# Kernel optimization log

Hardware: AMD Instinct MI355X
Metric: run time of the kernel (lower is better)

The kernel has to match this reference:

```python
import jax, jax.numpy as jnp
import numpy as np

EPS = 1e-5

def _ln(x, g, b):
    m = jnp.mean(x, axis=-1, keepdims=True)
    v = jnp.var(x, axis=-1, keepdims=True)
    return (x - m) * jax.lax.rsqrt(v + EPS) * g + b

def setup_inputs() -> dict:
    key = jax.random.key(0)
    ks = jax.random.split(key, 8)
    B, N, C, H = 2, 2048, 128, 8
    hid = 768
    s = lambda k, shp, fan: jax.random.normal(k, shp, jnp.float32) * (1.0 / np.sqrt(fan))
    return {
        "x1": jax.random.normal(ks[0], (B, N, C), jnp.float32),
        "x2": jax.random.normal(ks[1], (B, N, C), jnp.float32),
        "x3": jax.random.normal(ks[2], (B, N, C), jnp.float32),
        "ln1_g": jnp.ones((3, C), jnp.float32),
        "ln1_b": jnp.zeros((3, C), jnp.float32),
        "qkv_w": s(ks[3], (3, C, 3 * C), C),      # [branch, in, out]; torch Linear weight transposed
        "proj_w": s(ks[4], (3, C, C), C),
        "proj_b": jnp.zeros((3, C), jnp.float32),
        "ln2_g": jnp.ones((3 * C,), jnp.float32),
        "ln2_b": jnp.zeros((3 * C,), jnp.float32),
        "fc1_w": s(ks[5], (3 * C, hid), 3 * C),
        "fc1_b": jnp.zeros((hid,), jnp.float32),
        "fc2_w": s(ks[6], (hid, 3 * C), hid),
        "fc2_b": jnp.zeros((3 * C,), jnp.float32),
    }

def _branch(x, g, b, w_qkv, w_p, b_p, num_heads=8):
    B, N, C = x.shape
    hd = C // num_heads
    scale = hd ** -0.5
    xn = _ln(x, g, b)
    qkv = (xn @ w_qkv).reshape(B, N, 3, num_heads, hd)
    qkv = jnp.transpose(qkv, (2, 0, 3, 1, 4))  # [3,B,H,N,hd]
    q, k, v = qkv[0], qkv[1], qkv[2]
    attn = jax.nn.softmax(jnp.einsum('bhnd,bhmd->bhnm', q, k) * scale, axis=-1)
    o = jnp.einsum('bhnm,bhmd->bhnd', attn, v)
    o = jnp.transpose(o, (0, 2, 1, 3)).reshape(B, N, C)
    return x + (o @ w_p + b_p)

def reference(x1, x2, x3, ln1_g, ln1_b, qkv_w, proj_w, proj_b,
              ln2_g, ln2_b, fc1_w, fc1_b, fc2_w, fc2_b):
    xs = jnp.stack([x1, x2, x3])  # [3,B,N,C]
    xs = jax.vmap(_branch)(xs, ln1_g, ln1_b, qkv_w, proj_w, proj_b)
    B, N, C = x1.shape
    xc = jnp.transpose(xs, (1, 2, 0, 3)).reshape(B, N, 3 * C)  # concat(x1,x2,x3) on features
    h = jax.nn.gelu(_ln(xc, ln2_g, ln2_b) @ fc1_w + fc1_b, approximate=False)
    xc = xc + (h @ fc2_w + fc2_b)
    return xc[:, :, :C], xc[:, :, C:2 * C], xc[:, :, 2 * C:]
```

## Files before the change

kernel.cpp:

```cpp
#include <hip/hip_runtime.h>
#include <hip/hip_bf16.h>

typedef __hip_bfloat16 bf16;


static __device__ __forceinline__ float b2f(bf16 h) { return __bfloat162float(h); }
static __device__ __forceinline__ bf16 f2b(float f) { return __float2bfloat16(f); }
static __device__ __forceinline__ unsigned short f2bu(float f) {
    bf16 h = f2b(f);
    return *reinterpret_cast<unsigned short*>(&h);
}
static __device__ __forceinline__ float bs2f(short s) {
    return __uint_as_float(((unsigned)(unsigned short)s) << 16);
}

typedef __attribute__((ext_vector_type(8))) short short8;
typedef __attribute__((ext_vector_type(4))) short short4v;
typedef __attribute__((ext_vector_type(16))) float f32x16;
typedef __attribute__((ext_vector_type(2))) int int2v;

#define QSCALE 0.36067376022224085f

static __device__ __forceinline__ float xhalf(float x, int hi) {
    auto r = __builtin_amdgcn_permlane32_swap(__float_as_int(x), __float_as_int(x), false, false);
    return __int_as_float(hi ? r[0] : r[1]);
}

__global__ __launch_bounds__(256) void k_pre(const float* __restrict__ x1, const float* __restrict__ x2,
                                             const float* __restrict__ x3, const float* __restrict__ g,
                                             const float* __restrict__ b, bf16* __restrict__ xn,
                                             const float* __restrict__ qkv_w, const float* __restrict__ proj_w,
                                             const float* __restrict__ fc1_w, const float* __restrict__ fc2_w,
                                             bf16* __restrict__ wtq, bf16* __restrict__ wtp,
                                             bf16* __restrict__ wt1, bf16* __restrict__ wt2) {
    if (blockIdx.x >= 3072) {
        int idx = (blockIdx.x - 3072) * 256 + threadIdx.x;
        if (idx < 147456) {
            int bq = idx / 49152, i2 = idx % 49152;
            int n = i2 >> 7, k = i2 & 127;
            wtq[idx] = f2b(qkv_w[bq * 49152 + k * 384 + n]);
        } else if (idx < 196608) {
            int j = idx - 147456;
            int bq = j / 16384, i2 = j % 16384;
            int n = i2 >> 7, k = i2 & 127;
            wtp[j] = f2b(proj_w[bq * 16384 + k * 128 + n]);
        } else if (idx < 491520) {
            int j = idx - 196608;
            int n = j / 384, k = j - n * 384;
            wt1[j] = f2b(fc1_w[k * 768 + n]);
        } else {
            int j = idx - 491520;
            int n = j / 768, k = j - n * 768;
            wt2[j] = f2b(fc2_w[k * 384 + n]);
        }
        return;
    }
    int tid = threadIdx.x;
    int wave = tid >> 6, lane = tid & 63;
    int grow = blockIdx.x * 4 + wave;
    int branch = grow >> 12;
    const float* xp = (branch == 0) ? x1 : (branch == 1 ? x2 : x3);
    const float* row = xp + (size_t)(grow & 4095) * 128;
    float2 a = *reinterpret_cast<const float2*>(&row[2 * lane]);
    float s = a.x + a.y, sq = a.x * a.x + a.y * a.y;
#pragma unroll
    for (int off = 32; off >= 1; off >>= 1) { s += __shfl_xor(s, off); sq += __shfl_xor(sq, off); }
    float mean = s * (1.f / 128.f);
    float var = sq * (1.f / 128.f) - mean * mean;
    float rstd = rsqrtf(var + 1e-5f);
    float2 gv = *reinterpret_cast<const float2*>(&g[branch * 128 + 2 * lane]);
    float2 bv = *reinterpret_cast<const float2*>(&b[branch * 128 + 2 * lane]);
    bf16* orow = xn + (size_t)grow * 128;
    orow[2 * lane] = f2b((a.x - mean) * rstd * gv.x + bv.x);
    orow[2 * lane + 1] = f2b((a.y - mean) * rstd * gv.y + bv.y);
}

__device__ __forceinline__ f32x16 gemm_tile(const short* __restrict__ A, const short* __restrict__ W,
                                            int K, int rowbase, int colbase,
                                            short* als, short* wls) {
    int tid = threadIdx.x;
    int wid = tid >> 6, lane = tid & 63;
    int hi = lane >> 5, l31 = lane & 31;
    int wm = wid >> 1, wn = wid & 1;
    int sr = tid >> 3, skb = tid & 7;
    f32x16 acc;
#pragma unroll
    for (int i = 0; i < 16; ++i) acc[i] = 0.f;
    for (int k0 = 0; k0 < K; k0 += 64) {
        __syncthreads();
#pragma unroll
        for (int pass = 0; pass < 2; ++pass) {
            int r = sr + pass * 32;
            short8 av = *(const short8*)&A[(size_t)(rowbase + r) * K + k0 + skb * 8];
            *(short8*)&als[r * 64 + ((skb ^ (r & 7)) * 8)] = av;
            short8 wv = *(const short8*)&W[(size_t)(colbase + r) * K + k0 + skb * 8];
            *(short8*)&wls[r * 64 + ((skb ^ (r & 7)) * 8)] = wv;
        }
        __syncthreads();
#pragma unroll
        for (int ks = 0; ks < 4; ++ks) {
            int ra = wm * 32 + l31;
            int rb = wn * 32 + l31;
            int kb = ks * 2 + hi;
            short8 af = *(const short8*)&als[ra * 64 + ((kb ^ (ra & 7)) * 8)];
            short8 bf = *(const short8*)&wls[rb * 64 + ((kb ^ (rb & 7)) * 8)];
            acc = __builtin_amdgcn_mfma_f32_32x32x16_bf16(af, bf, acc, 0, 0, 0);
        }
    }
    return acc;
}

__global__ __launch_bounds__(256) void k_qkv_m(const bf16* __restrict__ xn, const bf16* __restrict__ wt,
                                               bf16* __restrict__ q, bf16* __restrict__ k, bf16* __restrict__ v) {
    __shared__ short als[64 * 64];
    __shared__ short wls[64 * 64];
    int branch = blockIdx.z;
    const short* A = (const short*)xn + (size_t)branch * 4096 * 128;
    const short* W = (const short*)wt + (size_t)branch * 384 * 128;
    int rowbase = blockIdx.x * 64, colbase = blockIdx.y * 64;
    f32x16 acc = gemm_tile(A, W, 128, rowbase, colbase, als, wls);
    int tid = threadIdx.x, wid = tid >> 6, lane = tid & 63;
    int hi = lane >> 5, l31 = lane & 31;
    int wm = wid >> 1, wn = wid & 1;
    int c = colbase + wn * 32 + l31;
    int which = c >> 7, h = (c >> 4) & 7, d = c & 15;
    if (which < 2) {
        bf16* dst = (which == 0) ? q : k;
        float scl = (which == 0) ? QSCALE : 1.0f;
#pragma unroll
        for (int i = 0; i < 16; ++i) {
            int mrow = (i & 3) + 8 * (i >> 2) + 4 * hi;
            int token = rowbase + wm * 32 + mrow;
            int bb = token >> 11, n = token & 2047;
            dst[((((size_t)branch * 2 + bb) * 8 + h) * 2048 + n) * 16 + d] = f2b(acc[i] * scl);
        }
    } else {
#pragma unroll
        for (int i = 0; i < 16; ++i) {
            int mrow = (i & 3) + 8 * (i >> 2) + 4 * hi;
            int token = rowbase + wm * 32 + mrow;
            int bb = token >> 11, n = token & 2047;
            size_t bh = (size_t)(branch * 2 + bb) * 8 + h;
            v[((bh * 32 + (n >> 6)) * 16 + d) * 64 + (n & 63)] = f2b(acc[i]);
        }
    }
}

__global__ __launch_bounds__(128, 4) void k_attn(const bf16* __restrict__ qg, const bf16* __restrict__ kg,
                                                 const bf16* __restrict__ vg, bf16* __restrict__ pacc,
                                                 float2* __restrict__ psm) {
    int bh = blockIdx.x;
    int qblk = blockIdx.y;
    int split = blockIdx.z;
    size_t base = (size_t)bh * (2048 * 16);
    size_t vtbase = (size_t)bh * 32768;
    int tid = threadIdx.x, wave = tid >> 6, lane = tid & 63;
    int hi = lane >> 5, l31 = lane & 31;
    int qrow = qblk * 64 + wave * 32 + l31;
    const short* qs = (const short*)qg;
    const short* ks = (const short*)kg;
    const short* vts = (const short*)vg;
    short8 qf = *(const short8*)&qs[base + (size_t)qrow * 16 + hi * 8];

    short8 one8;
#pragma unroll
    for (int j = 0; j < 8; ++j) one8[j] = (short)0x3F80;

    f32x16 acc;
    f32x16 negm;
#pragma unroll
    for (int r = 0; r < 16; ++r) { acc[r] = 0.f; negm[r] = -16.f; }
    float m = 16.f;

    int kbeg = split * 1024, kend = kbeg + 1024;

    for (int c0 = kbeg; c0 < kend; c0 += 64) {
        if (__any(acc[8] > 2.68435456e8f)) {
            int e = (__float_as_int(acc[8]) >> 23) - 127;
            int shift = e > 16 ? e - 16 : 0;
            float fac = __int_as_float((127 - shift) << 23);
            m += (float)shift;
#pragma unroll
            for (int r = 0; r < 16; ++r) negm[r] = -m;
#pragma unroll
            for (int r = 0; r < 16; ++r) acc[r] *= fac;
        }
        short8 kf0 = *(const short8*)&ks[base + (size_t)(c0 + l31) * 16 + hi * 8];
        short8 kf1 = *(const short8*)&ks[base + (size_t)(c0 + 32 + l31) * 16 + hi * 8];
        short8 vf1 = one8, vf2 = one8, vf3 = one8, vf4 = one8;
        if (l31 < 16) {
            const short* vt = &vts[vtbase + (size_t)(c0 >> 6) * 1024 + l31 * 64 + hi * 8];
            vf1 = *(const short8*)&vt[0];
            vf2 = *(const short8*)&vt[16];
            vf3 = *(const short8*)&vt[32];
            vf4 = *(const short8*)&vt[48];
        }
        f32x16 pa = __builtin_amdgcn_mfma_f32_32x32x16_bf16(kf0, qf, negm, 0, 0, 0);
        f32x16 pb = __builtin_amdgcn_mfma_f32_32x32x16_bf16(kf1, qf, negm, 0, 0, 0);
#pragma unroll
        for (int r = 0; r < 16; ++r) pa[r] = __builtin_amdgcn_exp2f(pa[r]);
#pragma unroll
        for (int r = 0; r < 16; ++r) pb[r] = __builtin_amdgcn_exp2f(pb[r]);
        unsigned wa[8], wb[8];
#pragma unroll
        for (int e = 0; e < 8; ++e) {
            unsigned t;
            asm("v_cvt_pk_bf16_f32 %0, %1, %2" : "=v"(t) : "v"(pa[2 * e]), "v"(pa[2 * e + 1]));
            wa[e] = t;
            asm("v_cvt_pk_bf16_f32 %0, %1, %2" : "=v"(t) : "v"(pb[2 * e]), "v"(pb[2 * e + 1]));
            wb[e] = t;
        }
        union { unsigned u[4]; short8 v; } b1, b2, b3, b4;
        {
            auto r0 = __builtin_amdgcn_permlane32_swap((int)wa[0], (int)wa[2], false, false);
            b1.u[0] = (unsigned)r0[0]; b1.u[2] = (unsigned)r0[1];
            auto r1 = __builtin_amdgcn_permlane32_swap((int)wa[1], (int)wa[3], false, false);
            b1.u[1] = (unsigned)r1[0]; b1.u[3] = (unsigned)r1[1];
            auto r2 = __builtin_amdgcn_permlane32_swap((int)wa[4], (int)wa[6], false, false);
            b2.u[0] = (unsigned)r2[0]; b2.u[2] = (unsigned)r2[1];
            auto r3 = __builtin_amdgcn_permlane32_swap((int)wa[5], (int)wa[7], false, false);
            b2.u[1] = (unsigned)r3[0]; b2.u[3] = (unsigned)r3[1];
            auto r4 = __builtin_amdgcn_permlane32_swap((int)wb[0], (int)wb[2], false, false);
            b3.u[0] = (unsigned)r4[0]; b3.u[2] = (unsigned)r4[1];
            auto r5 = __builtin_amdgcn_permlane32_swap((int)wb[1], (int)wb[3], false, false);
            b3.u[1] = (unsigned)r5[0]; b3.u[3] = (unsigned)r5[1];
            auto r6 = __builtin_amdgcn_permlane32_swap((int)wb[4], (int)wb[6], false, false);
            b4.u[0] = (unsigned)r6[0]; b4.u[2] = (unsigned)r6[1];
            auto r7 = __builtin_amdgcn_permlane32_swap((int)wb[5], (int)wb[7], false, false);
            b4.u[1] = (unsigned)r7[0]; b4.u[3] = (unsigned)r7[1];
        }
        acc = __builtin_amdgcn_mfma_f32_32x32x16_bf16(vf1, b1.v, acc, 0, 0, 0);
        acc = __builtin_amdgcn_mfma_f32_32x32x16_bf16(vf2, b2.v, acc, 0, 0, 0);
        acc = __builtin_amdgcn_mfma_f32_32x32x16_bf16(vf3, b3.v, acc, 0, 0, 0);
        acc = __builtin_amdgcn_mfma_f32_32x32x16_bf16(vf4, b4.v, acc, 0, 0, 0);
    }
    size_t pidx = ((size_t)(split * 48 + bh) * 2048 + qrow) * 16;
    unsigned u0 = (unsigned)f2bu(acc[0]) | ((unsigned)f2bu(acc[1]) << 16);
    unsigned u1 = (unsigned)f2bu(acc[2]) | ((unsigned)f2bu(acc[3]) << 16);
    unsigned u2 = (unsigned)f2bu(acc[4]) | ((unsigned)f2bu(acc[5]) << 16);
    unsigned u3 = (unsigned)f2bu(acc[6]) | ((unsigned)f2bu(acc[7]) << 16);
    short* pp = (short*)pacc;
    int2v w01; w01.x = (int)u0; w01.y = (int)u1;
    int2v w23; w23.x = (int)u2; w23.y = (int)u3;
    *(int2v*)&pp[pidx + 4 * hi] = w01;
    *(int2v*)&pp[pidx + 8 + 4 * hi] = w23;
    if (hi == 0) {
        float2 sm; sm.x = acc[8]; sm.y = m;
        psm[(size_t)(split * 48 + bh) * 2048 + qrow] = sm;
    }
}

__global__ __launch_bounds__(256) void k_proj_m(const bf16* __restrict__ pacc, const float2* __restrict__ psm,
                                                const bf16* __restrict__ wt, const float* __restrict__ pb,
                                                const float* __restrict__ x1, const float* __restrict__ x2,
                                                const float* __restrict__ x3, float* __restrict__ xc) {
    __shared__ short als[64 * 64];
    __shared__ short wls[64 * 64];
    int branch = blockIdx.z;
    const short* W = (const short*)wt + (size_t)branch * 128 * 128;
    const short* pp = (const short*)pacc;
    int rowbase = blockIdx.x * 64, colbase = blockIdx.y * 64;
    int tid = threadIdx.x;
    int wid = tid >> 6, lane = tid & 63;
    int hi = lane >> 5, l31 = lane & 31;
    int wm = wid >> 1, wn = wid & 1;
    int sr = tid >> 3, skb = tid & 7;
    f32x16 acc;
#pragma unroll
    for (int i = 0; i < 16; ++i) acc[i] = 0.f;
    for (int k0 = 0; k0 < 128; k0 += 64) {
        __syncthreads();
#pragma unroll
        for (int pass = 0; pass < 2; ++pass) {
            int r = sr + pass * 32;
            int row = rowbase + r;
            int bb = row >> 11, n = row & 2047;
            int h = (k0 >> 4) + (skb >> 1);
            int dlo = (skb & 1) * 8;
            size_t bh = (size_t)(branch * 2 + bb) * 8 + h;
            size_t ridx = bh * 2048 + n;
            float2 sm0 = psm[ridx];
            float2 sm1 = psm[(size_t)48 * 2048 + ridx];
            float mp = fmaxf(sm0.y, sm1.y);
            float w0 = __builtin_amdgcn_exp2f(sm0.y - mp);
            float w1 = __builtin_amdgcn_exp2f(sm1.y - mp);
            float inv = 1.f / (sm0.x * w0 + sm1.x * w1);
            w0 *= inv; w1 *= inv;
            short8 a0 = *(const short8*)&pp[ridx * 16 + dlo];
            short8 a1 = *(const short8*)&pp[((size_t)48 * 2048 + ridx) * 16 + dlo];
            short8 av;
#pragma unroll
            for (int j = 0; j < 8; ++j)
                av[j] = (short)f2bu(bs2f(a0[j]) * w0 + bs2f(a1[j]) * w1);
            *(short8*)&als[r * 64 + ((skb ^ (r & 7)) * 8)] = av;
            short8 wv = *(const short8*)&W[(size_t)(colbase + r) * 128 + k0 + skb * 8];
            *(short8*)&wls[r * 64 + ((skb ^ (r & 7)) * 8)] = wv;
        }
        __syncthreads();
#pragma unroll
        for (int ks = 0; ks < 4; ++ks) {
            int ra = wm * 32 + l31;
            int rb = wn * 32 + l31;
            int kb = ks * 2 + hi;
            short8 af = *(const short8*)&als[ra * 64 + ((kb ^ (ra & 7)) * 8)];
            short8 bf = *(const short8*)&wls[rb * 64 + ((kb ^ (rb & 7)) * 8)];
            acc = __builtin_amdgcn_mfma_f32_32x32x16_bf16(af, bf, acc, 0, 0, 0);
        }
    }
    int c = colbase + wn * 32 + l31;
    float bias = pb[branch * 128 + c];
    const float* xp = (branch == 0) ? x1 : (branch == 1 ? x2 : x3);
#pragma unroll
    for (int i = 0; i < 16; ++i) {
        int mrow = (i & 3) + 8 * (i >> 2) + 4 * hi;
        int row = rowbase + wm * 32 + mrow;
        xc[(size_t)row * 384 + branch * 128 + c] = acc[i] + bias + xp[(size_t)row * 128 + c];
    }
}

__global__ __launch_bounds__(256) void k_ln2(const float* __restrict__ xc, const float* __restrict__ g,
                                             const float* __restrict__ b, bf16* __restrict__ xcn) {
    int tid = threadIdx.x, wave = tid >> 6, lane = tid & 63;
    int row = blockIdx.x * 4 + wave;
    const float* rp = xc + (size_t)row * 384;
    float v[6];
    float s = 0.f, sq = 0.f;
#pragma unroll
    for (int i = 0; i < 6; ++i) {
        v[i] = rp[lane + i * 64];
        s += v[i]; sq += v[i] * v[i];
    }
#pragma unroll
    for (int off = 32; off >= 1; off >>= 1) { s += __shfl_xor(s, off); sq += __shfl_xor(sq, off); }
    float mean = s * (1.f / 384.f);
    float var = sq * (1.f / 384.f) - mean * mean;
    float rstd = rsqrtf(var + 1e-5f);
    bf16* op = xcn + (size_t)row * 384;
#pragma unroll
    for (int i = 0; i < 6; ++i) {
        int c = lane + i * 64;
        op[c] = f2b((v[i] - mean) * rstd * g[c] + b[c]);
    }
}

__global__ __launch_bounds__(256) void k_fc1_m(const bf16* __restrict__ xcn, const bf16* __restrict__ wt,
                                               const float* __restrict__ bias, bf16* __restrict__ h) {
    __shared__ short als[64 * 64];
    __shared__ short wls[64 * 64];
    const short* A = (const short*)xcn;
    const short* W = (const short*)wt;
    int rowbase = blockIdx.x * 64, colbase = blockIdx.y * 64;
    f32x16 acc = gemm_tile(A, W, 384, rowbase, colbase, als, wls);
    int tid = threadIdx.x, wid = tid >> 6, lane = tid & 63;
    int hi = lane >> 5, l31 = lane & 31;
    int wm = wid >> 1, wn = wid & 1;
    int c = colbase + wn * 32 + l31;
    float bs = bias[c];
#pragma unroll
    for (int i = 0; i < 16; ++i) {
        int mrow = (i & 3) + 8 * (i >> 2) + 4 * hi;
        int row = rowbase + wm * 32 + mrow;
        float vv = acc[i] + bs;
        float ge = 0.5f * vv * (1.f + erff(vv * 0.70710678118f));
        h[(size_t)row * 768 + c] = f2b(ge);
    }
}

__global__ __launch_bounds__(256) void k_fc2_m(const bf16* __restrict__ h, const bf16* __restrict__ wt,
                                               const float* __restrict__ bias, const float* __restrict__ xc,
                                               float* __restrict__ outp) {
    __shared__ short als[64 * 64];
    __shared__ short wls[64 * 64];
    const short* A = (const short*)h;
    const short* W = (const short*)wt;
    int rowbase = blockIdx.x * 64, colbase = blockIdx.y * 64;
    f32x16 acc = gemm_tile(A, W, 768, rowbase, colbase, als, wls);
    int tid = threadIdx.x, wid = tid >> 6, lane = tid & 63;
    int hi = lane >> 5, l31 = lane & 31;
    int wm = wid >> 1, wn = wid & 1;
    int c = colbase + wn * 32 + l31;
    float bs = bias[c];
    int which = c >> 7, cc = c & 127;
#pragma unroll
    for (int i = 0; i < 16; ++i) {
        int mrow = (i & 3) + 8 * (i >> 2) + 4 * hi;
        int row = rowbase + wm * 32 + mrow;
        outp[(size_t)which * 524288 + (size_t)row * 128 + cc] = acc[i] + bs + xc[(size_t)row * 384 + c];
    }
}

extern "C" void kernel_launch(void* const* d_in, const int* in_sizes, int n_in,
                              void* d_out, int out_size, void* d_ws, size_t ws_size,
                              hipStream_t stream) {
    const float* x1     = (const float*)d_in[0];
    const float* x2     = (const float*)d_in[1];
    const float* x3     = (const float*)d_in[2];
    const float* ln1_g  = (const float*)d_in[3];
    const float* ln1_b  = (const float*)d_in[4];
    const float* qkv_w  = (const float*)d_in[5];
    const float* proj_w = (const float*)d_in[6];
    const float* proj_b = (const float*)d_in[7];
    const float* ln2_g  = (const float*)d_in[8];
    const float* ln2_b  = (const float*)d_in[9];
    const float* fc1_w  = (const float*)d_in[10];
    const float* fc1_b  = (const float*)d_in[11];
    const float* fc2_w  = (const float*)d_in[12];
    const float* fc2_b  = (const float*)d_in[13];

    char* ws = (char*)d_ws;
    const size_t SB = 3145728;
    bf16* xn  = (bf16*)(ws + 0 * SB);
    bf16* qb  = (bf16*)(ws + 1 * SB);
    bf16* kb  = (bf16*)(ws + 2 * SB);
    bf16* vb  = (bf16*)(ws + 3 * SB);
    float* xc = (float*)(ws + 5 * SB);
    bf16* xcn = (bf16*)(ws + 5 * SB + 6291456);
    bf16* hb  = (bf16*)(ws + 6 * SB + 6291456);
    char* wbase = ws + 31457280;
    bf16* wtq = (bf16*)(wbase);
    bf16* wtp = (bf16*)(wbase + 294912);
    bf16* wt1 = (bf16*)(wbase + 393216);
    bf16* wt2 = (bf16*)(wbase + 983040);
    bf16*  pacc = (bf16*)(ws + 22020096);
    float2* psm = (float2*)(ws + 28311552);

    k_pre<<<6144, 256, 0, stream>>>(x1, x2, x3, ln1_g, ln1_b, xn,
                                    qkv_w, proj_w, fc1_w, fc2_w, wtq, wtp, wt1, wt2);
    k_qkv_m<<<dim3(64, 6, 3), 256, 0, stream>>>(xn, wtq, qb, kb, vb);
    k_attn<<<dim3(48, 32, 2), 128, 0, stream>>>(qb, kb, vb, pacc, psm);
    k_proj_m<<<dim3(64, 2, 3), 256, 0, stream>>>(pacc, psm, wtp, proj_b, x1, x2, x3, xc);
    k_ln2<<<1024, 256, 0, stream>>>(xc, ln2_g, ln2_b, xcn);
    k_fc1_m<<<dim3(64, 12, 1), 256, 0, stream>>>(xcn, wt1, fc1_b, hb);
    k_fc2_m<<<dim3(64, 6, 1), 256, 0, stream>>>(hb, wt2, fc2_b, xc, (float*)d_out);
}
```

Measured before the change: 95.05 us.

## Process two query tiles per attention block to reuse K/V loads

Each attention block now handles two 64-row query tiles (qblk and qblk+16) and shares every loaded K and V fragment between them through a factored helper. This halves the K/V global load traffic per query row and gives the scheduler two independent MFMA/exp chains to interleave. In exchange the grid is halved, register pressure roughly doubles, and launch bounds drop from 4 to 2 blocks per CU, which lowers occupancy.

```diff
diff --git a/kernel.cpp b/kernel.cpp
--- a/kernel.cpp
+++ b/kernel.cpp
@@ -20,11 +20,6 @@
 typedef __attribute__((ext_vector_type(2))) int int2v;
 
 #define QSCALE 0.36067376022224085f
-
-static __device__ __forceinline__ float xhalf(float x, int hi) {
-    auto r = __builtin_amdgcn_permlane32_swap(__float_as_int(x), __float_as_int(x), false, false);
-    return __int_as_float(hi ? r[0] : r[1]);
-}
 
 __global__ __launch_bounds__(256) void k_pre(const float* __restrict__ x1, const float* __restrict__ x2,
                                              const float* __restrict__ x3, const float* __restrict__ g,
@@ -146,7 +141,50 @@
     }
 }
 
-__global__ __launch_bounds__(128, 4) void k_attn(const bf16* __restrict__ qg, const bf16* __restrict__ kg,
+static __device__ __forceinline__ void attn_stream(short8 kf0, short8 kf1,
+                                                   short8 vf1, short8 vf2, short8 vf3, short8 vf4,
+                                                   short8 qf, const f32x16& negm, f32x16& acc) {
+    f32x16 pa = __builtin_amdgcn_mfma_f32_32x32x16_bf16(kf0, qf, negm, 0, 0, 0);
+    f32x16 pb = __builtin_amdgcn_mfma_f32_32x32x16_bf16(kf1, qf, negm, 0, 0, 0);
+#pragma unroll
+    for (int r = 0; r < 16; ++r) pa[r] = __builtin_amdgcn_exp2f(pa[r]);
+#pragma unroll
+    for (int r = 0; r < 16; ++r) pb[r] = __builtin_amdgcn_exp2f(pb[r]);
+    unsigned wa[8], wb[8];
+#pragma unroll
+    for (int e = 0; e < 8; ++e) {
+        unsigned t;
+        asm("v_cvt_pk_bf16_f32 %0, %1, %2" : "=v"(t) : "v"(pa[2 * e]), "v"(pa[2 * e + 1]));
+        wa[e] = t;
+        asm("v_cvt_pk_bf16_f32 %0, %1, %2" : "=v"(t) : "v"(pb[2 * e]), "v"(pb[2 * e + 1]));
+        wb[e] = t;
+    }
+    union { unsigned u[4]; short8 v; } b1, b2, b3, b4;
+    {
+        auto r0 = __builtin_amdgcn_permlane32_swap((int)wa[0], (int)wa[2], false, false);
+        b1.u[0] = (unsigned)r0[0]; b1.u[2] = (unsigned)r0[1];
+        auto r1 = __builtin_amdgcn_permlane32_swap((int)wa[1], (int)wa[3], false, false);
+        b1.u[1] = (unsigned)r1[0]; b1.u[3] = (unsigned)r1[1];
+        auto r2 = __builtin_amdgcn_permlane32_swap((int)wa[4], (int)wa[6], false, false);
+        b2.u[0] = (unsigned)r2[0]; b2.u[2] = (unsigned)r2[1];
+        auto r3 = __builtin_amdgcn_permlane32_swap((int)wa[5], (int)wa[7], false, false);
+        b2.u[1] = (unsigned)r3[0]; b2.u[3] = (unsigned)r3[1];
+        auto r4 = __builtin_amdgcn_permlane32_swap((int)wb[0], (int)wb[2], false, false);
+        b3.u[0] = (unsigned)r4[0]; b3.u[2] = (unsigned)r4[1];
+        auto r5 = __builtin_amdgcn_permlane32_swap((int)wb[1], (int)wb[3], false, false);
+        b3.u[1] = (unsigned)r5[0]; b3.u[3] = (unsigned)r5[1];
+        auto r6 = __builtin_amdgcn_permlane32_swap((int)wb[4], (int)wb[6], false, false);
+        b4.u[0] = (unsigned)r6[0]; b4.u[2] = (unsigned)r6[1];
+        auto r7 = __builtin_amdgcn_permlane32_swap((int)wb[5], (int)wb[7], false, false);
+        b4.u[1] = (unsigned)r7[0]; b4.u[3] = (unsigned)r7[1];
+    }
+    acc = __builtin_amdgcn_mfma_f32_32x32x16_bf16(vf1, b1.v, acc, 0, 0, 0);
+    acc = __builtin_amdgcn_mfma_f32_32x32x16_bf16(vf2, b2.v, acc, 0, 0, 0);
+    acc = __builtin_amdgcn_mfma_f32_32x32x16_bf16(vf3, b3.v, acc, 0, 0, 0);
+    acc = __builtin_amdgcn_mfma_f32_32x32x16_bf16(vf4, b4.v, acc, 0, 0, 0);
+}
+
+__global__ __launch_bounds__(128, 2) void k_attn(const bf16* __restrict__ qg, const bf16* __restrict__ kg,
                                                  const bf16* __restrict__ vg, bf16* __restrict__ pacc,
                                                  float2* __restrict__ psm) {
     int bh = blockIdx.x;
@@ -156,34 +194,45 @@
     size_t vtbase = (size_t)bh * 32768;
     int tid = threadIdx.x, wave = tid >> 6, lane = tid & 63;
     int hi = lane >> 5, l31 = lane & 31;
-    int qrow = qblk * 64 + wave * 32 + l31;
+    int qrowA = qblk * 64 + wave * 32 + l31;
+    int qrowB = (qblk + 16) * 64 + wave * 32 + l31;
     const short* qs = (const short*)qg;
     const short* ks = (const short*)kg;
     const short* vts = (const short*)vg;
-    short8 qf = *(const short8*)&qs[base + (size_t)qrow * 16 + hi * 8];
+    short8 qfA = *(const short8*)&qs[base + (size_t)qrowA * 16 + hi * 8];
+    short8 qfB = *(const short8*)&qs[base + (size_t)qrowB * 16 + hi * 8];
 
     short8 one8;
 #pragma unroll
     for (int j = 0; j < 8; ++j) one8[j] = (short)0x3F80;
 
-    f32x16 acc;
-    f32x16 negm;
-#pragma unroll
-    for (int r = 0; r < 16; ++r) { acc[r] = 0.f; negm[r] = -16.f; }
-    float m = 16.f;
+    f32x16 accA, accB, negmA, negmB;
+#pragma unroll
+    for (int r = 0; r < 16; ++r) { accA[r] = 0.f; accB[r] = 0.f; negmA[r] = -16.f; negmB[r] = -16.f; }
+    float mA = 16.f, mB = 16.f;
 
     int kbeg = split * 1024, kend = kbeg + 1024;
 
     for (int c0 = kbeg; c0 < kend; c0 += 64) {
-        if (__any(acc[8] > 2.68435456e8f)) {
-            int e = (__float_as_int(acc[8]) >> 23) - 127;
+        if (__any(accA[8] > 2.68435456e8f)) {
+            int e = (__float_as_int(accA[8]) >> 23) - 127;
             int shift = e > 16 ? e - 16 : 0;
             float fac = __int_as_float((127 - shift) << 23);
-            m += (float)shift;
-#pragma unroll
-            for (int r = 0; r < 16; ++r) negm[r] = -m;
-#pragma unroll
-            for (int r = 0; r < 16; ++r) acc[r] *= fac;
+            mA += (float)shift;
+#pragma unroll
+            for (int r = 0; r < 16; ++r) negmA[r] = -mA;
+#pragma unroll
+            for (int r = 0; r < 16; ++r) accA[r] *= fac;
+        }
+        if (__any(accB[8] > 2.68435456e8f)) {
+            int e = (__float_as_int(accB[8]) >> 23) - 127;
+            int shift = e > 16 ? e - 16 : 0;
+            float fac = __int_as_float((127 - shift) << 23);
+            mB += (float)shift;
+#pragma unroll
+            for (int r = 0; r < 16; ++r) negmB[r] = -mB;
+#pragma unroll
+            for (int r = 0; r < 16; ++r) accB[r] *= fac;
         }
         short8 kf0 = *(const short8*)&ks[base + (size_t)(c0 + l31) * 16 + hi * 8];
         short8 kf1 = *(const short8*)&ks[base + (size_t)(c0 + 32 + l31) * 16 + hi * 8];
@@ -195,58 +244,39 @@
             vf3 = *(const short8*)&vt[32];
             vf4 = *(const short8*)&vt[48];
         }
-        f32x16 pa = __builtin_amdgcn_mfma_f32_32x32x16_bf16(kf0, qf, negm, 0, 0, 0);
-        f32x16 pb = __builtin_amdgcn_mfma_f32_32x32x16_bf16(kf1, qf, negm, 0, 0, 0);
-#pragma unroll
-        for (int r = 0; r < 16; ++r) pa[r] = __builtin_amdgcn_exp2f(pa[r]);
-#pragma unroll
-        for (int r = 0; r < 16; ++r) pb[r] = __builtin_amdgcn_exp2f(pb[r]);
-        unsigned wa[8], wb[8];
-#pragma unroll
-        for (int e = 0; e < 8; ++e) {
-            unsigned t;
-            asm("v_cvt_pk_bf16_f32 %0, %1, %2" : "=v"(t) : "v"(pa[2 * e]), "v"(pa[2 * e + 1]));
-            wa[e] = t;
-            asm("v_cvt_pk_bf16_f32 %0, %1, %2" : "=v"(t) : "v"(pb[2 * e]), "v"(pb[2 * e + 1]));
-            wb[e] = t;
-        }
-        union { unsigned u[4]; short8 v; } b1, b2, b3, b4;
-        {
-            auto r0 = __builtin_amdgcn_permlane32_swap((int)wa[0], (int)wa[2], false, false);
-            b1.u[0] = (unsigned)r0[0]; b1.u[2] = (unsigned)r0[1];
-            auto r1 = __builtin_amdgcn_permlane32_swap((int)wa[1], (int)wa[3], false, false);
-            b1.u[1] = (unsigned)r1[0]; b1.u[3] = (unsigned)r1[1];
-            auto r2 = __builtin_amdgcn_permlane32_swap((int)wa[4], (int)wa[6], false, false);
-            b2.u[0] = (unsigned)r2[0]; b2.u[2] = (unsigned)r2[1];
-            auto r3 = __builtin_amdgcn_permlane32_swap((int)wa[5], (int)wa[7], false, false);
-            b2.u[1] = (unsigned)r3[0]; b2.u[3] = (unsigned)r3[1];
-            auto r4 = __builtin_amdgcn_permlane32_swap((int)wb[0], (int)wb[2], false, false);
-            b3.u[0] = (unsigned)r4[0]; b3.u[2] = (unsigned)r4[1];
-            auto r5 = __builtin_amdgcn_permlane32_swap((int)wb[1], (int)wb[3], false, false);
-            b3.u[1] = (unsigned)r5[0]; b3.u[3] = (unsigned)r5[1];
-            auto r6 = __builtin_amdgcn_permlane32_swap((int)wb[4], (int)wb[6], false, false);
-            b4.u[0] = (unsigned)r6[0]; b4.u[2] = (unsigned)r6[1];
-            auto r7 = __builtin_amdgcn_permlane32_swap((int)wb[5], (int)wb[7], false, false);
-            b4.u[1] = (unsigned)r7[0]; b4.u[3] = (unsigned)r7[1];
-        }
-        acc = __builtin_amdgcn_mfma_f32_32x32x16_bf16(vf1, b1.v, acc, 0, 0, 0);
-        acc = __builtin_amdgcn_mfma_f32_32x32x16_bf16(vf2, b2.v, acc, 0, 0, 0);
-        acc = __builtin_amdgcn_mfma_f32_32x32x16_bf16(vf3, b3.v, acc, 0, 0, 0);
-        acc = __builtin_amdgcn_mfma_f32_32x32x16_bf16(vf4, b4.v, acc, 0, 0, 0);
-    }
-    size_t pidx = ((size_t)(split * 48 + bh) * 2048 + qrow) * 16;
-    unsigned u0 = (unsigned)f2bu(acc[0]) | ((unsigned)f2bu(acc[1]) << 16);
-    unsigned u1 = (unsigned)f2bu(acc[2]) | ((unsigned)f2bu(acc[3]) << 16);
-    unsigned u2 = (unsigned)f2bu(acc[4]) | ((unsigned)f2bu(acc[5]) << 16);
-    unsigned u3 = (unsigned)f2bu(acc[6]) | ((unsigned)f2bu(acc[7]) << 16);
+        attn_stream(kf0, kf1, vf1, vf2, vf3, vf4, qfA, negmA, accA);
+        attn_stream(kf0, kf1, vf1, vf2, vf3, vf4, qfB, negmB, accB);
+    }
     short* pp = (short*)pacc;
-    int2v w01; w01.x = (int)u0; w01.y = (int)u1;
-    int2v w23; w23.x = (int)u2; w23.y = (int)u3;
-    *(int2v*)&pp[pidx + 4 * hi] = w01;
-    *(int2v*)&pp[pidx + 8 + 4 * hi] = w23;
-    if (hi == 0) {
-        float2 sm; sm.x = acc[8]; sm.y = m;
-        psm[(size_t)(split * 48 + bh) * 2048 + qrow] = sm;
+    {
+        size_t pidx = ((size_t)(split * 48 + bh) * 2048 + qrowA) * 16;
+        unsigned u0 = (unsigned)f2bu(accA[0]) | ((unsigned)f2bu(accA[1]) << 16);
+        unsigned u1 = (unsigned)f2bu(accA[2]) | ((unsigned)f2bu(accA[3]) << 16);
+        unsigned u2 = (unsigned)f2bu(accA[4]) | ((unsigned)f2bu(accA[5]) << 16);
+        unsigned u3 = (unsigned)f2bu(accA[6]) | ((unsigned)f2bu(accA[7]) << 16);
+        int2v w01; w01.x = (int)u0; w01.y = (int)u1;
+        int2v w23; w23.x = (int)u2; w23.y = (int)u3;
+        *(int2v*)&pp[pidx + 4 * hi] = w01;
+        *(int2v*)&pp[pidx + 8 + 4 * hi] = w23;
+        if (hi == 0) {
+            float2 sm; sm.x = accA[8]; sm.y = mA;
+            psm[(size_t)(split * 48 + bh) * 2048 + qrowA] = sm;
+        }
+    }
+    {
+        size_t pidx = ((size_t)(split * 48 + bh) * 2048 + qrowB) * 16;
+        unsigned u0 = (unsigned)f2bu(accB[0]) | ((unsigned)f2bu(accB[1]) << 16);
+        unsigned u1 = (unsigned)f2bu(accB[2]) | ((unsigned)f2bu(accB[3]) << 16);
+        unsigned u2 = (unsigned)f2bu(accB[4]) | ((unsigned)f2bu(accB[5]) << 16);
+        unsigned u3 = (unsigned)f2bu(accB[6]) | ((unsigned)f2bu(accB[7]) << 16);
+        int2v w01; w01.x = (int)u0; w01.y = (int)u1;
+        int2v w23; w23.x = (int)u2; w23.y = (int)u3;
+        *(int2v*)&pp[pidx + 4 * hi] = w01;
+        *(int2v*)&pp[pidx + 8 + 4 * hi] = w23;
+        if (hi == 0) {
+            float2 sm; sm.x = accB[8]; sm.y = mB;
+            psm[(size_t)(split * 48 + bh) * 2048 + qrowB] = sm;
+        }
     }
 }
 
@@ -427,7 +457,7 @@
     k_pre<<<6144, 256, 0, stream>>>(x1, x2, x3, ln1_g, ln1_b, xn,
                                     qkv_w, proj_w, fc1_w, fc2_w, wtq, wtp, wt1, wt2);
     k_qkv_m<<<dim3(64, 6, 3), 256, 0, stream>>>(xn, wtq, qb, kb, vb);
-    k_attn<<<dim3(48, 32, 2), 128, 0, stream>>>(qb, kb, vb, pacc, psm);
+    k_attn<<<dim3(48, 16, 2), 128, 0, stream>>>(qb, kb, vb, pacc, psm);
     k_proj_m<<<dim3(64, 2, 3), 256, 0, stream>>>(pacc, psm, wtp, proj_b, x1, x2, x3, xc);
     k_ln2<<<1024, 256, 0, stream>>>(xc, ln2_g, ln2_b, xcn);
     k_fc1_m<<<dim3(64, 12, 1), 256, 0, stream>>>(xcn, wt1, fc1_b, hb);
```

Result: faster. 84.80 us (-10.8%).
